# Kernel tuning notes

Hardware: AMD Instinct MI355X
Metric: run time of the kernel (lower is better)

The kernel has to match this reference:

```python
import jax, jax.numpy as jnp
import numpy as np

N = 50000
IN_DIM = 512
HID = 64
E = 800000


def setup_inputs() -> dict:
    key = jax.random.key(0)
    k1, k2, k3, k4 = jax.random.split(key, 4)
    x = jax.random.normal(k1, (N, IN_DIM), dtype=jnp.float32)
    edge_index = jax.random.randint(k2, (2, E), 0, N, dtype=jnp.int32)
    # Glorot-ish init for linear weights
    W1 = jax.random.normal(k3, (IN_DIM, HID), dtype=jnp.float32) / np.sqrt(IN_DIM)
    b1 = jnp.zeros((HID,), dtype=jnp.float32)
    W2 = jax.random.normal(k4, (HID, HID), dtype=jnp.float32) / np.sqrt(HID)
    b2 = jnp.zeros((HID,), dtype=jnp.float32)
    return {"x": x, "edge_index": edge_index, "W1": W1, "b1": b1, "W2": W2, "b2": b2}


def gcn_conv(x, src, dst, norm, W, b, n):
    # x' = D^{-1/2} (A+I) D^{-1/2} x W + b  (PyG GCNConv with self-loops)
    h = x @ W                                  # [N, out] dense GEMM
    msg = h[src] * norm[:, None]               # gather + scale per edge
    out = jax.ops.segment_sum(msg, dst, num_segments=n)  # scatter-add
    return out + b


def reference(x, edge_index, W1, b1, W2, b2):
    n = x.shape[0]
    loop = jnp.arange(n, dtype=edge_index.dtype)
    src = jnp.concatenate([edge_index[0], loop])  # add self-loops
    dst = jnp.concatenate([edge_index[1], loop])
    deg = jax.ops.segment_sum(jnp.ones_like(src, dtype=x.dtype), dst, num_segments=n)
    dinv = jnp.where(deg > 0, jax.lax.rsqrt(deg), 0.0)
    norm = dinv[src] * dinv[dst]               # symmetric normalization per edge
    h = gcn_conv(x, src, dst, norm, W1, b1, n)
    h = jax.nn.relu(h)
    # dropout is identity in eval mode (reference baseline)
    z = gcn_conv(h, src, dst, norm, W2, b2, n)
    return z
```

## Files before the change

### kernel.cpp

```cpp
#include <hip/hip_runtime.h>
#include <stdint.h>


typedef __attribute__((ext_vector_type(8))) short short8;
typedef __attribute__((ext_vector_type(4))) float f32x4;

#define SLOTS 64

__device__ __forceinline__ uint32_t bf16_rne(float f) {
  uint32_t u = __float_as_uint(f);
  return (u + 0x7FFFu + ((u >> 16) & 1u)) >> 16;
}

__global__ __launch_bounds__(256) void fill_kernel(const int* __restrict__ src,
                                                   const int* __restrict__ dst, int E,
                                                   int* __restrict__ cursor,
                                                   int* __restrict__ meta) {
  int i = blockIdx.x * 256 + threadIdx.x;
  if (i < E) {
    int s = src[i];
    int d = dst[i];
    int pos = atomicAdd(&cursor[d], 1);
    if (pos < SLOTS) meta[(size_t)d * SLOTS + pos] = s + 1;
  }
}

__global__ __launch_bounds__(256) void dinv_kernel(const int* __restrict__ cursor,
                                                   float* __restrict__ dinv, int n) {
  int i = blockIdx.x * 256 + threadIdx.x;
  if (i < n) dinv[i] = rsqrtf((float)(cursor[i] + 1));
}

__global__ __launch_bounds__(256) void wfrag_kernel(const float* __restrict__ W1,
                                                    const float* __restrict__ W2,
                                                    short8* __restrict__ wh1,
                                                    short8* __restrict__ wl1,
                                                    short8* __restrict__ wh2,
                                                    short8* __restrict__ wl2,
                                                    int K1, int K2) {
  int idx = blockIdx.x * 256 + threadIdx.x;
  int tot1 = (K1 >> 5) * 256;
  int tot2 = (K2 >> 5) * 256;
  const float* W;
  short8 *wh, *wl;
  if (idx < tot1) {
    W = W1; wh = wh1; wl = wl1;
  } else if (idx < tot1 + tot2) {
    idx -= tot1;
    W = W2; wh = wh2; wl = wl2;
  } else {
    return;
  }
  int lane = idx & 63;
  int ct = (idx >> 6) & 3;
  int kt = idx >> 8;
  int m = lane & 15, q = lane >> 4;
  int col = ct * 16 + m;
  short8 h, l;
#pragma unroll
  for (int j = 0; j < 8; ++j) {
    float f = W[(size_t)(kt * 32 + q * 8 + j) * 64 + col];
    uint32_t hb = bf16_rne(f);
    float hf = __uint_as_float(hb << 16);
    float lo = f - hf;
    h[j] = (short)hb;
    l[j] = (short)bf16_rne(lo);
  }
  wh[idx] = h;
  wl[idx] = l;
}

__global__ __launch_bounds__(256) void gemm_mfma_kernel(const float* __restrict__ A,
                                                        const short8* __restrict__ wh,
                                                        const short8* __restrict__ wl,
                                                        ushort* __restrict__ outb,
                                                        int n, int K) {
  const int t = threadIdx.x;
  const int lane = t & 63;
  const int m = lane & 15, q = lane >> 4;
  const int row0 = blockIdx.x * 128 + (t >> 6) * 32;
  int r0 = row0 + m;
  int r1 = row0 + 16 + m;
  if (r0 >= n) r0 = n - 1;
  if (r1 >= n) r1 = n - 1;
  const float* ap0 = A + (size_t)r0 * K + q * 8;
  const float* ap1 = A + (size_t)r1 * K + q * 8;
  const short8* whp = wh + lane;
  const short8* wlp = wl + lane;
  const int nkt = K >> 5;
  f32x4 acc[2][4];
#pragma unroll
  for (int g = 0; g < 2; ++g)
#pragma unroll
    for (int c = 0; c < 4; ++c) acc[g][c] = 0.f;

  float4 xa0 = *(const float4*)(ap0);
  float4 xa1 = *(const float4*)(ap0 + 4);
  float4 xb0 = *(const float4*)(ap1);
  float4 xb1 = *(const float4*)(ap1 + 4);
  short8 bh[4] = {whp[0], whp[64], whp[128], whp[192]};
  short8 bl[4] = {wlp[0], wlp[64], wlp[128], wlp[192]};

  auto cvt = [&](const float4& u0, const float4& u1, short8& hi, short8& lo) {
    float xf[8] = {u0.x, u0.y, u0.z, u0.w, u1.x, u1.y, u1.z, u1.w};
#pragma unroll
    for (int j = 0; j < 8; ++j) {
      uint32_t hb = bf16_rne(xf[j]);
      float hf = __uint_as_float(hb << 16);
      hi[j] = (short)hb;
      lo[j] = (short)bf16_rne(xf[j] - hf);
    }
  };
  auto compute = [&]() {
    short8 ah0, al0, ah1, al1;
    cvt(xa0, xa1, ah0, al0);
    cvt(xb0, xb1, ah1, al1);
#pragma unroll
    for (int c = 0; c < 4; ++c) {
      acc[0][c] = __builtin_amdgcn_mfma_f32_16x16x32_bf16(ah0, bh[c], acc[0][c], 0, 0, 0);
      acc[1][c] = __builtin_amdgcn_mfma_f32_16x16x32_bf16(ah1, bh[c], acc[1][c], 0, 0, 0);
    }
#pragma unroll
    for (int c = 0; c < 4; ++c) {
      acc[0][c] = __builtin_amdgcn_mfma_f32_16x16x32_bf16(ah0, bl[c], acc[0][c], 0, 0, 0);
      acc[1][c] = __builtin_amdgcn_mfma_f32_16x16x32_bf16(ah1, bl[c], acc[1][c], 0, 0, 0);
    }
#pragma unroll
    for (int c = 0; c < 4; ++c) {
      acc[0][c] = __builtin_amdgcn_mfma_f32_16x16x32_bf16(al0, bh[c], acc[0][c], 0, 0, 0);
      acc[1][c] = __builtin_amdgcn_mfma_f32_16x16x32_bf16(al1, bh[c], acc[1][c], 0, 0, 0);
    }
  };

  for (int kt = 0; kt < nkt - 1; ++kt) {
    const float* an0 = ap0 + 32;
    const float* an1 = ap1 + 32;
    float4 nxa0 = *(const float4*)(an0);
    float4 nxa1 = *(const float4*)(an0 + 4);
    float4 nxb0 = *(const float4*)(an1);
    float4 nxb1 = *(const float4*)(an1 + 4);
    const short8* whn = whp + 256;
    const short8* wln = wlp + 256;
    short8 nh[4] = {whn[0], whn[64], whn[128], whn[192]};
    short8 nl[4] = {wln[0], wln[64], wln[128], wln[192]};
    compute();
    xa0 = nxa0; xa1 = nxa1; xb0 = nxb0; xb1 = nxb1;
#pragma unroll
    for (int c = 0; c < 4; ++c) { bh[c] = nh[c]; bl[c] = nl[c]; }
    ap0 = an0; ap1 = an1; whp = whn; wlp = wln;
  }
  compute();

#pragma unroll
  for (int g = 0; g < 2; ++g)
#pragma unroll
    for (int i = 0; i < 4; ++i) {
      int rr = row0 + g * 16 + q * 4 + i;
      if (rr < n) {
        ushort* op = outb + (size_t)rr * 64 + m;
        op[0]  = (ushort)bf16_rne(acc[g][0][i]);
        op[16] = (ushort)bf16_rne(acc[g][1][i]);
        op[32] = (ushort)bf16_rne(acc[g][2][i]);
        op[48] = (ushort)bf16_rne(acc[g][3][i]);
      }
    }
}

__global__ __launch_bounds__(256) void agg_kernel(const ushort* __restrict__ H,
                                                  const int* __restrict__ deg,
                                                  const int* __restrict__ meta,
                                                  const float* __restrict__ dinv,
                                                  const float* __restrict__ bias,
                                                  float* __restrict__ out, int n, int do_relu) {
  const int t = threadIdx.x;
  const int sl = t & 7;
  const int v = blockIdx.x * 32 + (t >> 3);
  if (v >= n) return;
  const float dv = dinv[v];
  const float dvv = dv * dv;
  float acc[8];
  {
    uint4 hv = *(const uint4*)&H[(size_t)v * 64 + (sl << 3)];
    uint32_t u[4] = {hv.x, hv.y, hv.z, hv.w};
#pragma unroll
    for (int j = 0; j < 4; ++j) {
      acc[2 * j]     = __uint_as_float(u[j] << 16) * dvv;
      acc[2 * j + 1] = __uint_as_float(u[j] & 0xFFFF0000u) * dvv;
    }
  }
  int dg = deg[v];
  if (dg > SLOTS) dg = SLOTS;
  int nc = (dg + 7) >> 3;
  const int4* p = (const int4*)(meta + (size_t)v * SLOTS);

  int4 ma0, ma1, mb0, mb1;
  uint4 ra[8], rb[8];
  float wa[8], wb[8];
  auto gath = [&](int4 c0, int4 c1, uint4* r, float* wr) {
    int u[8] = {c0.x, c0.y, c0.z, c0.w, c1.x, c1.y, c1.z, c1.w};
#pragma unroll
    for (int j = 0; j < 8; ++j) {
      int idx = (u[j] > 0) ? (u[j] - 1) : 0;
      r[j] = *(const uint4*)&H[(size_t)idx * 64 + (sl << 3)];
      wr[j] = dinv[idx];
    }
  };
  auto consume = [&](int4 c0, int4 c1, const uint4* r, const float* wr) {
    int u[8] = {c0.x, c0.y, c0.z, c0.w, c1.x, c1.y, c1.z, c1.w};
#pragma unroll
    for (int j = 0; j < 8; ++j) {
      const float wgt = (u[j] > 0) ? wr[j] * dv : 0.f;
      uint32_t q[4] = {r[j].x, r[j].y, r[j].z, r[j].w};
#pragma unroll
      for (int k = 0; k < 4; ++k) {
        acc[2 * k]     = fmaf(__uint_as_float(q[k] << 16), wgt, acc[2 * k]);
        acc[2 * k + 1] = fmaf(__uint_as_float(q[k] & 0xFFFF0000u), wgt, acc[2 * k + 1]);
      }
    }
  };

  if (nc > 0) {
    ma0 = p[0]; ma1 = p[1];
    gath(ma0, ma1, ra, wa);
  }
  for (int c = 0; c < nc - 1; ++c) {
    mb0 = p[2 * c + 2]; mb1 = p[2 * c + 3];
    gath(mb0, mb1, rb, wb);
    consume(ma0, ma1, ra, wa);
    ma0 = mb0; ma1 = mb1;
#pragma unroll
    for (int j = 0; j < 8; ++j) { ra[j] = rb[j]; wa[j] = wb[j]; }
  }
  if (nc > 0) consume(ma0, ma1, ra, wa);

  const float4 blo = *(const float4*)&bias[sl << 3];
  const float4 bhi = *(const float4*)&bias[(sl << 3) + 4];
  float bb[8] = {blo.x, blo.y, blo.z, blo.w, bhi.x, bhi.y, bhi.z, bhi.w};
#pragma unroll
  for (int j = 0; j < 8; ++j) {
    acc[j] += bb[j];
    if (do_relu) acc[j] = fmaxf(acc[j], 0.f);
  }
  float* op = out + (size_t)v * 64 + (sl << 3);
  *(float4*)op = make_float4(acc[0], acc[1], acc[2], acc[3]);
  *(float4*)(op + 4) = make_float4(acc[4], acc[5], acc[6], acc[7]);
}

extern "C" void kernel_launch(void* const* d_in, const int* in_sizes, int n_in,
                              void* d_out, int out_size, void* d_ws, size_t ws_size,
                              hipStream_t stream) {
  const float* x = (const float*)d_in[0];
  const int* ei = (const int*)d_in[1];
  const float* W1 = (const float*)d_in[2];
  const float* b1 = (const float*)d_in[3];
  const float* W2 = (const float*)d_in[4];
  const float* b2 = (const float*)d_in[5];
  float* out = (float*)d_out;

  const int HID = in_sizes[3];
  const int IN_DIM = in_sizes[2] / HID;
  const int N = in_sizes[0] / IN_DIM;
  const int E = in_sizes[1] / 2;

  uint8_t* p = (uint8_t*)d_ws;
  auto alloc = [&](size_t bytes) {
    void* r = (void*)p;
    p += (bytes + 255) & ~(size_t)255;
    return r;
  };
  int* meta = (int*)alloc((size_t)N * SLOTS * 4);
  int* cursor = (int*)alloc((size_t)N * 4);
  float* dinv = (float*)alloc((size_t)N * 4);
  ushort* hb = (ushort*)alloc((size_t)N * HID * 2);
  float* h = (float*)alloc((size_t)N * HID * 4);
  short8* wh1 = (short8*)alloc((size_t)(IN_DIM >> 5) * 256 * 16);
  short8* wl1 = (short8*)alloc((size_t)(IN_DIM >> 5) * 256 * 16);
  short8* wh2 = (short8*)alloc((size_t)(HID >> 5) * 256 * 16);
  short8* wl2 = (short8*)alloc((size_t)(HID >> 5) * 256 * 16);

  const int* srcp = ei;
  const int* dstp = ei + E;

  const size_t zspan = (size_t)((uint8_t*)(cursor + N) - (uint8_t*)meta);
  hipMemsetAsync(meta, 0, zspan, stream);
  fill_kernel<<<(E + 255) / 256, 256, 0, stream>>>(srcp, dstp, E, cursor, meta);
  dinv_kernel<<<(N + 255) / 256, 256, 0, stream>>>(cursor, dinv, N);

  const int wtot = (IN_DIM >> 5) * 256 + (HID >> 5) * 256;
  wfrag_kernel<<<(wtot + 255) / 256, 256, 0, stream>>>(W1, W2, wh1, wl1, wh2, wl2,
                                                       IN_DIM, HID);

  gemm_mfma_kernel<<<(N + 127) / 128, 256, 0, stream>>>(x, wh1, wl1, hb, N, IN_DIM);
  agg_kernel<<<(N + 31) / 32, 256, 0, stream>>>(hb, cursor, meta, dinv, b1, h, N, 1);
  gemm_mfma_kernel<<<(N + 127) / 128, 256, 0, stream>>>(h, wh2, wl2, hb, N, HID);
  agg_kernel<<<(N + 31) / 32, 256, 0, stream>>>(hb, cursor, meta, dinv, b2, out, N, 0);
}
```

Baseline: 268.7 us.

## Merge setup kernels, skip meta memset, halve GEMM tile rows, use nontemporal loads

New measurement: 283.6 us. 5.6% more time.

```diff
diff --git a/kernel.cpp b/kernel.cpp
--- a/kernel.cpp
+++ b/kernel.cpp
@@ -12,32 +12,23 @@
   return (u + 0x7FFFu + ((u >> 16) & 1u)) >> 16;
 }
 
-__global__ __launch_bounds__(256) void fill_kernel(const int* __restrict__ src,
-                                                   const int* __restrict__ dst, int E,
-                                                   int* __restrict__ cursor,
-                                                   int* __restrict__ meta) {
-  int i = blockIdx.x * 256 + threadIdx.x;
-  if (i < E) {
-    int s = src[i];
-    int d = dst[i];
-    int pos = atomicAdd(&cursor[d], 1);
-    if (pos < SLOTS) meta[(size_t)d * SLOTS + pos] = s + 1;
-  }
-}
-
-__global__ __launch_bounds__(256) void dinv_kernel(const int* __restrict__ cursor,
-                                                   float* __restrict__ dinv, int n) {
-  int i = blockIdx.x * 256 + threadIdx.x;
-  if (i < n) dinv[i] = rsqrtf((float)(cursor[i] + 1));
-}
-
-__global__ __launch_bounds__(256) void wfrag_kernel(const float* __restrict__ W1,
-                                                    const float* __restrict__ W2,
-                                                    short8* __restrict__ wh1,
-                                                    short8* __restrict__ wl1,
-                                                    short8* __restrict__ wh2,
-                                                    short8* __restrict__ wl2,
-                                                    int K1, int K2) {
+__global__ __launch_bounds__(256) void fill_wfrag_kernel(
+    const int* __restrict__ src, const int* __restrict__ dst, int E,
+    int* __restrict__ cursor, int* __restrict__ meta,
+    const float* __restrict__ W1, const float* __restrict__ W2,
+    short8* __restrict__ wh1, short8* __restrict__ wl1,
+    short8* __restrict__ wh2, short8* __restrict__ wl2,
+    int K1, int K2, int wblocks) {
+  if ((int)blockIdx.x >= wblocks) {
+    int i = (blockIdx.x - wblocks) * 256 + threadIdx.x;
+    if (i < E) {
+      int s = __builtin_nontemporal_load(src + i);
+      int d = __builtin_nontemporal_load(dst + i);
+      int pos = atomicAdd(&cursor[d], 1);
+      if (pos < SLOTS) meta[(size_t)d * SLOTS + pos] = s;
+    }
+    return;
+  }
   int idx = blockIdx.x * 256 + threadIdx.x;
   int tot1 = (K1 >> 5) * 256;
   int tot2 = (K2 >> 5) * 256;
@@ -70,39 +61,37 @@
   wl[idx] = l;
 }
 
-__global__ __launch_bounds__(256) void gemm_mfma_kernel(const float* __restrict__ A,
-                                                        const short8* __restrict__ wh,
-                                                        const short8* __restrict__ wl,
-                                                        ushort* __restrict__ outb,
-                                                        int n, int K) {
+__global__ __launch_bounds__(256) void gemm_mfma_kernel(
+    const float* __restrict__ A, const short8* __restrict__ wh,
+    const short8* __restrict__ wl, ushort* __restrict__ outb, int n, int K,
+    int gblocks, const int* __restrict__ cursor, float* __restrict__ dinv,
+    int ndinv) {
+  if ((int)blockIdx.x >= gblocks) {
+    int i = (blockIdx.x - gblocks) * 256 + threadIdx.x;
+    if (i < ndinv) dinv[i] = rsqrtf((float)(cursor[i] + 1));
+    return;
+  }
   const int t = threadIdx.x;
   const int lane = t & 63;
   const int m = lane & 15, q = lane >> 4;
-  const int row0 = blockIdx.x * 128 + (t >> 6) * 32;
+  const int row0 = blockIdx.x * 64 + (t >> 6) * 16;
   int r0 = row0 + m;
-  int r1 = row0 + 16 + m;
   if (r0 >= n) r0 = n - 1;
-  if (r1 >= n) r1 = n - 1;
-  const float* ap0 = A + (size_t)r0 * K + q * 8;
-  const float* ap1 = A + (size_t)r1 * K + q * 8;
+  const float* ap = A + (size_t)r0 * K + q * 8;
   const short8* whp = wh + lane;
   const short8* wlp = wl + lane;
   const int nkt = K >> 5;
-  f32x4 acc[2][4];
-#pragma unroll
-  for (int g = 0; g < 2; ++g)
-#pragma unroll
-    for (int c = 0; c < 4; ++c) acc[g][c] = 0.f;
-
-  float4 xa0 = *(const float4*)(ap0);
-  float4 xa1 = *(const float4*)(ap0 + 4);
-  float4 xb0 = *(const float4*)(ap1);
-  float4 xb1 = *(const float4*)(ap1 + 4);
+  f32x4 acc[4];
+#pragma unroll
+  for (int c = 0; c < 4; ++c) acc[c] = 0.f;
+
+  f32x4 xa0 = __builtin_nontemporal_load((const f32x4*)ap);
+  f32x4 xa1 = __builtin_nontemporal_load((const f32x4*)(ap + 4));
   short8 bh[4] = {whp[0], whp[64], whp[128], whp[192]};
   short8 bl[4] = {wlp[0], wlp[64], wlp[128], wlp[192]};
 
-  auto cvt = [&](const float4& u0, const float4& u1, short8& hi, short8& lo) {
-    float xf[8] = {u0.x, u0.y, u0.z, u0.w, u1.x, u1.y, u1.z, u1.w};
+  auto cvt = [&](const f32x4& u0, const f32x4& u1, short8& hi, short8& lo) {
+    float xf[8] = {u0[0], u0[1], u0[2], u0[3], u1[0], u1[1], u1[2], u1[3]};
 #pragma unroll
     for (int j = 0; j < 8; ++j) {
       uint32_t hb = bf16_rne(xf[j]);
@@ -112,58 +101,46 @@
     }
   };
   auto compute = [&]() {
-    short8 ah0, al0, ah1, al1;
-    cvt(xa0, xa1, ah0, al0);
-    cvt(xb0, xb1, ah1, al1);
-#pragma unroll
-    for (int c = 0; c < 4; ++c) {
-      acc[0][c] = __builtin_amdgcn_mfma_f32_16x16x32_bf16(ah0, bh[c], acc[0][c], 0, 0, 0);
-      acc[1][c] = __builtin_amdgcn_mfma_f32_16x16x32_bf16(ah1, bh[c], acc[1][c], 0, 0, 0);
-    }
-#pragma unroll
-    for (int c = 0; c < 4; ++c) {
-      acc[0][c] = __builtin_amdgcn_mfma_f32_16x16x32_bf16(ah0, bl[c], acc[0][c], 0, 0, 0);
-      acc[1][c] = __builtin_amdgcn_mfma_f32_16x16x32_bf16(ah1, bl[c], acc[1][c], 0, 0, 0);
-    }
-#pragma unroll
-    for (int c = 0; c < 4; ++c) {
-      acc[0][c] = __builtin_amdgcn_mfma_f32_16x16x32_bf16(al0, bh[c], acc[0][c], 0, 0, 0);
-      acc[1][c] = __builtin_amdgcn_mfma_f32_16x16x32_bf16(al1, bh[c], acc[1][c], 0, 0, 0);
-    }
+    short8 ah, al;
+    cvt(xa0, xa1, ah, al);
+#pragma unroll
+    for (int c = 0; c < 4; ++c)
+      acc[c] = __builtin_amdgcn_mfma_f32_16x16x32_bf16(ah, bh[c], acc[c], 0, 0, 0);
+#pragma unroll
+    for (int c = 0; c < 4; ++c)
+      acc[c] = __builtin_amdgcn_mfma_f32_16x16x32_bf16(ah, bl[c], acc[c], 0, 0, 0);
+#pragma unroll
+    for (int c = 0; c < 4; ++c)
+      acc[c] = __builtin_amdgcn_mfma_f32_16x16x32_bf16(al, bh[c], acc[c], 0, 0, 0);
   };
 
   for (int kt = 0; kt < nkt - 1; ++kt) {
-    const float* an0 = ap0 + 32;
-    const float* an1 = ap1 + 32;
-    float4 nxa0 = *(const float4*)(an0);
-    float4 nxa1 = *(const float4*)(an0 + 4);
-    float4 nxb0 = *(const float4*)(an1);
-    float4 nxb1 = *(const float4*)(an1 + 4);
+    const float* an = ap + 32;
+    f32x4 nxa0 = __builtin_nontemporal_load((const f32x4*)an);
+    f32x4 nxa1 = __builtin_nontemporal_load((const f32x4*)(an + 4));
     const short8* whn = whp + 256;
     const short8* wln = wlp + 256;
     short8 nh[4] = {whn[0], whn[64], whn[128], whn[192]};
     short8 nl[4] = {wln[0], wln[64], wln[128], wln[192]};
     compute();
-    xa0 = nxa0; xa1 = nxa1; xb0 = nxb0; xb1 = nxb1;
+    xa0 = nxa0; xa1 = nxa1;
 #pragma unroll
     for (int c = 0; c < 4; ++c) { bh[c] = nh[c]; bl[c] = nl[c]; }
-    ap0 = an0; ap1 = an1; whp = whn; wlp = wln;
+    ap = an; whp = whn; wlp = wln;
   }
   compute();
 
 #pragma unroll
-  for (int g = 0; g < 2; ++g)
-#pragma unroll
-    for (int i = 0; i < 4; ++i) {
-      int rr = row0 + g * 16 + q * 4 + i;
-      if (rr < n) {
-        ushort* op = outb + (size_t)rr * 64 + m;
-        op[0]  = (ushort)bf16_rne(acc[g][0][i]);
-        op[16] = (ushort)bf16_rne(acc[g][1][i]);
-        op[32] = (ushort)bf16_rne(acc[g][2][i]);
-        op[48] = (ushort)bf16_rne(acc[g][3][i]);
-      }
-    }
+  for (int i = 0; i < 4; ++i) {
+    int rr = row0 + q * 4 + i;
+    if (rr < n) {
+      ushort* op = outb + (size_t)rr * 64 + m;
+      op[0]  = (ushort)bf16_rne(acc[0][i]);
+      op[16] = (ushort)bf16_rne(acc[1][i]);
+      op[32] = (ushort)bf16_rne(acc[2][i]);
+      op[48] = (ushort)bf16_rne(acc[3][i]);
+    }
+  }
 }
 
 __global__ __launch_bounds__(256) void agg_kernel(const ushort* __restrict__ H,
@@ -171,7 +148,8 @@
                                                   const int* __restrict__ meta,
                                                   const float* __restrict__ dinv,
                                                   const float* __restrict__ bias,
-                                                  float* __restrict__ out, int n, int do_relu) {
+                                                  float* __restrict__ out, int n,
+                                                  int do_relu) {
   const int t = threadIdx.x;
   const int sl = t & 7;
   const int v = blockIdx.x * 32 + (t >> 3);
@@ -200,16 +178,16 @@
     int u[8] = {c0.x, c0.y, c0.z, c0.w, c1.x, c1.y, c1.z, c1.w};
 #pragma unroll
     for (int j = 0; j < 8; ++j) {
-      int idx = (u[j] > 0) ? (u[j] - 1) : 0;
+      unsigned idx = (unsigned)u[j];
+      if (idx >= (unsigned)n) idx = 0;
       r[j] = *(const uint4*)&H[(size_t)idx * 64 + (sl << 3)];
       wr[j] = dinv[idx];
     }
   };
-  auto consume = [&](int4 c0, int4 c1, const uint4* r, const float* wr) {
-    int u[8] = {c0.x, c0.y, c0.z, c0.w, c1.x, c1.y, c1.z, c1.w};
+  auto consume = [&](int rem, const uint4* r, const float* wr) {
 #pragma unroll
     for (int j = 0; j < 8; ++j) {
-      const float wgt = (u[j] > 0) ? wr[j] * dv : 0.f;
+      const float wgt = (j < rem) ? wr[j] * dv : 0.f;
       uint32_t q[4] = {r[j].x, r[j].y, r[j].z, r[j].w};
 #pragma unroll
       for (int k = 0; k < 4; ++k) {
@@ -226,12 +204,12 @@
   for (int c = 0; c < nc - 1; ++c) {
     mb0 = p[2 * c + 2]; mb1 = p[2 * c + 3];
     gath(mb0, mb1, rb, wb);
-    consume(ma0, ma1, ra, wa);
+    consume(dg - (c << 3), ra, wa);
     ma0 = mb0; ma1 = mb1;
 #pragma unroll
     for (int j = 0; j < 8; ++j) { ra[j] = rb[j]; wa[j] = wb[j]; }
   }
-  if (nc > 0) consume(ma0, ma1, ra, wa);
+  if (nc > 0) consume(dg - ((nc - 1) << 3), ra, wa);
 
   const float4 blo = *(const float4*)&bias[sl << 3];
   const float4 bhi = *(const float4*)&bias[(sl << 3) + 4];
@@ -242,8 +220,15 @@
     if (do_relu) acc[j] = fmaxf(acc[j], 0.f);
   }
   float* op = out + (size_t)v * 64 + (sl << 3);
-  *(float4*)op = make_float4(acc[0], acc[1], acc[2], acc[3]);
-  *(float4*)(op + 4) = make_float4(acc[4], acc[5], acc[6], acc[7]);
+  f32x4 v0 = {acc[0], acc[1], acc[2], acc[3]};
+  f32x4 v1 = {acc[4], acc[5], acc[6], acc[7]};
+  if (do_relu) {
+    *(f32x4*)op = v0;
+    *(f32x4*)(op + 4) = v1;
+  } else {
+    __builtin_nontemporal_store(v0, (f32x4*)op);
+    __builtin_nontemporal_store(v1, (f32x4*)(op + 4));
+  }
 }
 
 extern "C" void kernel_launch(void* const* d_in, const int* in_sizes, int n_in,
@@ -281,17 +266,20 @@
   const int* srcp = ei;
   const int* dstp = ei + E;
 
-  const size_t zspan = (size_t)((uint8_t*)(cursor + N) - (uint8_t*)meta);
-  hipMemsetAsync(meta, 0, zspan, stream);
-  fill_kernel<<<(E + 255) / 256, 256, 0, stream>>>(srcp, dstp, E, cursor, meta);
-  dinv_kernel<<<(N + 255) / 256, 256, 0, stream>>>(cursor, dinv, N);
+  (void)hipMemsetAsync(cursor, 0, (size_t)N * 4, stream);
 
   const int wtot = (IN_DIM >> 5) * 256 + (HID >> 5) * 256;
-  wfrag_kernel<<<(wtot + 255) / 256, 256, 0, stream>>>(W1, W2, wh1, wl1, wh2, wl2,
-                                                       IN_DIM, HID);
-
-  gemm_mfma_kernel<<<(N + 127) / 128, 256, 0, stream>>>(x, wh1, wl1, hb, N, IN_DIM);
+  const int wblocks = (wtot + 255) / 256;
+  const int fblocks = (E + 255) / 256;
+  fill_wfrag_kernel<<<wblocks + fblocks, 256, 0, stream>>>(
+      srcp, dstp, E, cursor, meta, W1, W2, wh1, wl1, wh2, wl2, IN_DIM, HID, wblocks);
+
+  const int g1 = (N + 63) / 64;
+  const int dblk = (N + 255) / 256;
+  gemm_mfma_kernel<<<g1 + dblk, 256, 0, stream>>>(x, wh1, wl1, hb, N, IN_DIM, g1,
+                                                  cursor, dinv, N);
   agg_kernel<<<(N + 31) / 32, 256, 0, stream>>>(hb, cursor, meta, dinv, b1, h, N, 1);
-  gemm_mfma_kernel<<<(N + 127) / 128, 256, 0, stream>>>(h, wh2, wl2, hb, N, HID);
+  gemm_mfma_kernel<<<g1, 256, 0, stream>>>(h, wh2, wl2, hb, N, HID, g1,
+                                           cursor, dinv, 0);
   agg_kernel<<<(N + 31) / 32, 256, 0, stream>>>(hb, cursor, meta, dinv, b2, out, N, 0);
 }
```
